# Optimization experiments

Measured on AMD Instinct MI355X. Metric: run time of the kernel, lower is better.

The kernel has to match this reference:

```python
import jax, jax.numpy as jnp
import numpy as np
import math

HEAD_SIZE = 64

def setup_inputs() -> dict:
    key = jax.random.key(0)
    k1, k2, k3 = jax.random.split(key, 3)
    B, nh, T, hs = 2, 16, 2048, HEAD_SIZE
    return {
        "query": jax.random.normal(k1, (B, nh, T, hs), dtype=jnp.float32),
        "key": jax.random.normal(k2, (B, nh, T, hs), dtype=jnp.float32),
        "value": jax.random.normal(k3, (B, nh, T, hs), dtype=jnp.float32),
        "attention_mask": jnp.zeros((B, 1, 1, T), dtype=jnp.float32),
    }

def reference(query, key, value, attention_mask):
    scale = 1.0 / math.sqrt(HEAD_SIZE)
    # [B, nh, T, T] scores
    scores = jnp.einsum("bhqd,bhkd->bhqk", query, key) * scale
    scores = scores + attention_mask
    attn = jax.nn.softmax(scores, axis=-1)
    # [B, nh, T, hs]
    return jnp.einsum("bhqk,bhkd->bhqd", attn, value)
```

## Files before the change

kernel.cpp:

```cpp
#include <hip/hip_runtime.h>
#include <hip/hip_bf16.h>

#define TSEQ 2048
#define DH   64
#define NBH  32
#define KT   32
#define NIT  32

typedef __attribute__((ext_vector_type(8)))  short short8_t;
typedef __attribute__((ext_vector_type(16))) float f32x16;
typedef __attribute__((ext_vector_type(4)))  unsigned short ushort4_t;

#define LOG2E 1.44269504088896340736f
#define MSUB  12.0f

__device__ __forceinline__ unsigned short f2bf(float f) {
    unsigned int u = __float_as_uint(f);
    return (unsigned short)((u + 0x7fffu + ((u >> 16) & 1u)) >> 16);
}

__device__ __forceinline__ unsigned int cvtpk(float lo, float hi) {
    unsigned int r;
    asm("v_cvt_pk_bf16_f32 %0, %1, %2" : "=v"(r) : "v"(lo), "v"(hi));
    return r;
}

__device__ __forceinline__ float exp2r(float x) {
#if __has_builtin(__builtin_amdgcn_exp2f)
    return __builtin_amdgcn_exp2f(x);
#else
    return exp2f(x);
#endif
}

#define GL2L16(g, l) __builtin_amdgcn_global_load_lds( \
    (__attribute__((address_space(1))) void*)(void*)(g), \
    (__attribute__((address_space(3))) void*)(l), 16, 0, 0)

__device__ __forceinline__ unsigned int kswz(unsigned int row, unsigned int cb) {
    return row * 128u + (cb ^ ((row & 7u) << 4));
}
__device__ __forceinline__ unsigned int vswz(unsigned int row, unsigned int cb) {
    return row * 64u + (cb ^ (((row >> 1) & 3u) << 4));
}

__global__ __launch_bounds__(256) void prep_kernel(const float* __restrict__ K,
                                                   unsigned short* __restrict__ Kb,
                                                   const float* __restrict__ V,
                                                   unsigned short* __restrict__ Vt) {
    __shared__ float tile[64][65];
    const int tid = threadIdx.x;
    if (blockIdx.x < 2048) {
        int i = blockIdx.x * 256 + tid;
        const float4* s = reinterpret_cast<const float4*>(K) + (size_t)i * 2;
        float4 a = s[0], b = s[1];
        short8_t o;
        o[0] = (short)f2bf(a.x); o[1] = (short)f2bf(a.y);
        o[2] = (short)f2bf(a.z); o[3] = (short)f2bf(a.w);
        o[4] = (short)f2bf(b.x); o[5] = (short)f2bf(b.y);
        o[6] = (short)f2bf(b.z); o[7] = (short)f2bf(b.w);
        *reinterpret_cast<short8_t*>(Kb + (size_t)i * 8) = o;
        return;
    }
    const int vbid = blockIdx.x - 2048;
    const int bh = vbid >> 5;
    const int t0 = (vbid & 31) * 64;
    const float* src = V + ((size_t)bh * TSEQ + t0) * DH;
#pragma unroll
    for (int it = 0; it < 4; ++it) {
        int idx = tid + it * 256;
        int row = idx >> 4;
        int c   = (idx & 15) * 4;
        float4 v = *reinterpret_cast<const float4*>(src + row * DH + c);
        tile[row][c + 0] = v.x; tile[row][c + 1] = v.y;
        tile[row][c + 2] = v.z; tile[row][c + 3] = v.w;
    }
    __syncthreads();
#pragma unroll
    for (int it = 0; it < 4; ++it) {
        int idx = tid + it * 256;
        int d  = idx >> 4;
        int c  = (idx & 15) * 4;
        ushort4_t o;
        o[0] = f2bf(tile[c + 0][d]); o[1] = f2bf(tile[c + 1][d]);
        o[2] = f2bf(tile[c + 2][d]); o[3] = f2bf(tile[c + 3][d]);
        *reinterpret_cast<ushort4_t*>(Vt + ((size_t)bh * DH + d) * TSEQ + t0 + c) = o;
    }
}

__global__ __launch_bounds__(256, 2) void attn_kernel(const float* __restrict__ Qf,
                                                      const unsigned short* __restrict__ Kb,
                                                      const unsigned short* __restrict__ Vt,
                                                      const float* __restrict__ mask,
                                                      float* __restrict__ out) {
    __shared__ char lds[40960];
    float* smsk = reinterpret_cast<float*>(lds + 32768);

    const int tid  = threadIdx.x;
    const int wave = tid >> 6;
    const int lane = tid & 63;
    const int l31  = lane & 31;
    const int hi   = lane >> 5;
    const int s    = wave >> 1;
    const int qw   = wave & 1;

    const int bid = blockIdx.x;
    const int bh  = (bid & 7) * 4 + (bid >> 7);
    const int qb  = (bid >> 3) & 15;
    const int q0  = qb * 128 + qw * 64;
    const int b   = bh >> 4;

    const char* gKc = reinterpret_cast<const char*>(Kb + (size_t)bh * TSEQ * DH);
    const char* gVc = reinterpret_cast<const char*>(Vt + (size_t)bh * DH * TSEQ);
    const unsigned int kr  = wave * 8 + (lane >> 3);
    const unsigned int kcb = (lane & 7) * 16;
    const unsigned int vd  = wave * 16 + (lane >> 2);
    const unsigned int vcb = (lane & 3) * 16;
    const char* p0 = gKc + (size_t)kr * 128 + (kcb ^ ((kr & 7u) << 4));
    const char* p1 = p0 + (size_t)1024 * 128;
    const char* p2 = gVc + (size_t)vd * 4096 + (vcb ^ (((vd >> 1) & 3u) << 4));
    const char* p3 = p2 + (size_t)1024 * 2;
    const unsigned int lo0 = (wave +  0) * 1024 + lane * 16;
    const unsigned int lo1 = (wave +  4) * 1024 + lane * 16;
    const unsigned int lo2 = (wave +  8) * 1024 + lane * 16;
    const unsigned int lo3 = (wave + 12) * 1024 + lane * 16;

    auto stage = [&](int buf) {
        char* base = lds + buf * 16384;
        GL2L16(p0, base + lo0);
        GL2L16(p1, base + lo1);
        GL2L16(p2, base + lo2);
        GL2L16(p3, base + lo3);
        p0 += KT * 128; p1 += KT * 128; p2 += KT * 2; p3 += KT * 2;
    };

    stage(0);
    stage(1);

    {
        const float4* m4 = reinterpret_cast<const float4*>(mask + (size_t)b * TSEQ);
        float4* s4 = reinterpret_cast<float4*>(smsk);
#pragma unroll
        for (int i = 0; i < 2; ++i) {
            int idx = tid + i * 256;
            float4 v = m4[idx];
            float4 w;
            w.x = v.x * LOG2E - MSUB; w.y = v.y * LOG2E - MSUB;
            w.z = v.z * LOG2E - MSUB; w.w = v.w * LOG2E - MSUB;
            s4[idx] = w;
        }
    }

    const float QS = 0.125f * LOG2E;
    short8_t qfA[4], qfB[4];
#pragma unroll
    for (int qs = 0; qs < 2; ++qs) {
        const float* qrow = Qf + ((size_t)bh * TSEQ + q0 + qs * 32 + l31) * DH;
#pragma unroll
        for (int dc = 0; dc < 4; ++dc) {
            float4 v0 = *reinterpret_cast<const float4*>(qrow + 16 * dc + 8 * hi);
            float4 v1 = *reinterpret_cast<const float4*>(qrow + 16 * dc + 8 * hi + 4);
            union { unsigned int u[4]; short8_t s8; } pk;
            pk.u[0] = cvtpk(v0.x * QS, v0.y * QS);
            pk.u[1] = cvtpk(v0.z * QS, v0.w * QS);
            pk.u[2] = cvtpk(v1.x * QS, v1.y * QS);
            pk.u[3] = cvtpk(v1.z * QS, v1.w * QS);
            if (qs == 0) qfA[dc] = pk.s8; else qfB[dc] = pk.s8;
        }
    }

    f32x16 oA0, oA1, oB0, oB1;
#pragma unroll
    for (int r = 0; r < 16; ++r) { oA0[r] = 0.f; oA1[r] = 0.f; oB0[r] = 0.f; oB1[r] = 0.f; }
    float lA = 0.f, lB = 0.f;

    const char* const cKbase = lds + s * 4096;
    const char* const cVbase = lds + 8192 + s * 4096;
    const int kofs = s * 1024;

    auto do_tile = [&](int cur, int it) {
        const char* cK = cKbase + cur * 16384;
        const char* cV = cVbase + cur * 16384;

        short8_t kf0 = *reinterpret_cast<const short8_t*>(cK + kswz(l31, 16 * hi));
        short8_t kf1 = *reinterpret_cast<const short8_t*>(cK + kswz(l31, 32 + 16 * hi));
        short8_t kf2 = *reinterpret_cast<const short8_t*>(cK + kswz(l31, 64 + 16 * hi));
        short8_t kf3 = *reinterpret_cast<const short8_t*>(cK + kswz(l31, 96 + 16 * hi));

        const float* mb = &smsk[kofs + it * KT + 4 * hi];
        float4 mv0 = *reinterpret_cast<const float4*>(mb);
        float4 mv1 = *reinterpret_cast<const float4*>(mb + 8);
        float4 mv2 = *reinterpret_cast<const float4*>(mb + 16);
        float4 mv3 = *reinterpret_cast<const float4*>(mb + 24);
        f32x16 scA;
        scA[0]  = mv0.x; scA[1]  = mv0.y; scA[2]  = mv0.z; scA[3]  = mv0.w;
        scA[4]  = mv1.x; scA[5]  = mv1.y; scA[6]  = mv1.z; scA[7]  = mv1.w;
        scA[8]  = mv2.x; scA[9]  = mv2.y; scA[10] = mv2.z; scA[11] = mv2.w;
        scA[12] = mv3.x; scA[13] = mv3.y; scA[14] = mv3.z; scA[15] = mv3.w;
        f32x16 scB = scA;

        __builtin_amdgcn_s_setprio(1);
        scA = __builtin_amdgcn_mfma_f32_32x32x16_bf16(kf0, qfA[0], scA, 0, 0, 0);
        scB = __builtin_amdgcn_mfma_f32_32x32x16_bf16(kf0, qfB[0], scB, 0, 0, 0);
        scA = __builtin_amdgcn_mfma_f32_32x32x16_bf16(kf1, qfA[1], scA, 0, 0, 0);
        scB = __builtin_amdgcn_mfma_f32_32x32x16_bf16(kf1, qfB[1], scB, 0, 0, 0);
        scA = __builtin_amdgcn_mfma_f32_32x32x16_bf16(kf2, qfA[2], scA, 0, 0, 0);
        scB = __builtin_amdgcn_mfma_f32_32x32x16_bf16(kf2, qfB[2], scB, 0, 0, 0);
        scA = __builtin_amdgcn_mfma_f32_32x32x16_bf16(kf3, qfA[3], scA, 0, 0, 0);
        scB = __builtin_amdgcn_mfma_f32_32x32x16_bf16(kf3, qfB[3], scB, 0, 0, 0);
        __builtin_amdgcn_s_setprio(0);

        short8_t vf00 = *reinterpret_cast<const short8_t*>(cV + vswz(l31,      16 * hi));
        short8_t vf01 = *reinterpret_cast<const short8_t*>(cV + vswz(32 + l31, 16 * hi));
        short8_t vf10 = *reinterpret_cast<const short8_t*>(cV + vswz(l31,      32 + 16 * hi));
        short8_t vf11 = *reinterpret_cast<const short8_t*>(cV + vswz(32 + l31, 32 + 16 * hi));

#pragma unroll
        for (int c = 0; c < 2; ++c) {
            unsigned int a0, a1, a2, a3, b0, b1, b2, b3;
            {
                float e0 = exp2r(scA[8*c+0]), e1 = exp2r(scA[8*c+1]);
                float e2 = exp2r(scA[8*c+2]), e3 = exp2r(scA[8*c+3]);
                float e4 = exp2r(scA[8*c+4]), e5 = exp2r(scA[8*c+5]);
                float e6 = exp2r(scA[8*c+6]), e7 = exp2r(scA[8*c+7]);
                lA += ((e0+e1)+(e2+e3)) + ((e4+e5)+(e6+e7));
                a0 = cvtpk(e0, e1); a2 = cvtpk(e2, e3);
                a1 = cvtpk(e4, e5); a3 = cvtpk(e6, e7);
            }
            {
                float e0 = exp2r(scB[8*c+0]), e1 = exp2r(scB[8*c+1]);
                float e2 = exp2r(scB[8*c+2]), e3 = exp2r(scB[8*c+3]);
                float e4 = exp2r(scB[8*c+4]), e5 = exp2r(scB[8*c+5]);
                float e6 = exp2r(scB[8*c+6]), e7 = exp2r(scB[8*c+7]);
                lB += ((e0+e1)+(e2+e3)) + ((e4+e5)+(e6+e7));
                b0 = cvtpk(e0, e1); b2 = cvtpk(e2, e3);
                b1 = cvtpk(e4, e5); b3 = cvtpk(e6, e7);
            }
            asm("v_permlane32_swap_b32 %0, %1" : "+v"(a0), "+v"(a1));
            asm("v_permlane32_swap_b32 %0, %1" : "+v"(a2), "+v"(a3));
            asm("v_permlane32_swap_b32 %0, %1" : "+v"(b0), "+v"(b1));
            asm("v_permlane32_swap_b32 %0, %1" : "+v"(b2), "+v"(b3));
            union { unsigned int u[4]; short8_t s8; } pfA, pfB;
            pfA.u[0] = a0; pfA.u[1] = a2; pfA.u[2] = a1; pfA.u[3] = a3;
            pfB.u[0] = b0; pfB.u[1] = b2; pfB.u[2] = b1; pfB.u[3] = b3;
            short8_t vf0 = c ? vf10 : vf00;
            short8_t vf1 = c ? vf11 : vf01;
            __builtin_amdgcn_s_setprio(1);
            oA0 = __builtin_amdgcn_mfma_f32_32x32x16_bf16(vf0, pfA.s8, oA0, 0, 0, 0);
            oB0 = __builtin_amdgcn_mfma_f32_32x32x16_bf16(vf0, pfB.s8, oB0, 0, 0, 0);
            oA1 = __builtin_amdgcn_mfma_f32_32x32x16_bf16(vf1, pfA.s8, oA1, 0, 0, 0);
            oB1 = __builtin_amdgcn_mfma_f32_32x32x16_bf16(vf1, pfB.s8, oB1, 0, 0, 0);
            __builtin_amdgcn_s_setprio(0);
        }
    };

    __syncthreads();

    for (int t = 0; t < NIT - 1; ++t) {
        asm volatile("s_waitcnt vmcnt(4)" ::: "memory");
        __builtin_amdgcn_s_barrier();
        __builtin_amdgcn_sched_barrier(0);
        do_tile(t & 1, t);
        __builtin_amdgcn_sched_barrier(0);
        __builtin_amdgcn_s_barrier();
        __builtin_amdgcn_sched_barrier(0);
        if (t < NIT - 2) stage(t & 1);
    }
    asm volatile("s_waitcnt vmcnt(0)" ::: "memory");
    __builtin_amdgcn_s_barrier();
    __builtin_amdgcn_sched_barrier(0);
    do_tile((NIT - 1) & 1, NIT - 1);

    __syncthreads();

    float lAt = lA + __shfl_xor(lA, 32);
    float lBt = lB + __shfl_xor(lB, 32);
    if (s == 1) {
#pragma unroll
        for (int qs = 0; qs < 2; ++qs) {
            char* wp = lds + qw * 16384 + qs * 8192;
            const f32x16& o0 = qs ? oB0 : oA0;
            const f32x16& o1 = qs ? oB1 : oA1;
#pragma unroll
            for (int i = 0; i < 8; ++i) {
                float4 v;
                if (i < 4) { v.x = o0[4*i]; v.y = o0[4*i+1]; v.z = o0[4*i+2]; v.w = o0[4*i+3]; }
                else       { v.x = o1[4*(i-4)]; v.y = o1[4*(i-4)+1]; v.z = o1[4*(i-4)+2]; v.w = o1[4*(i-4)+3]; }
                *reinterpret_cast<float4*>(wp + lane * 128 + ((i * 16) ^ ((lane & 7u) << 4))) = v;
            }
        }
        if (hi == 0) {
            reinterpret_cast<float*>(lds + 32768 + (qw * 2 + 0) * 128)[l31] = lAt;
            reinterpret_cast<float*>(lds + 32768 + (qw * 2 + 1) * 128)[l31] = lBt;
        }
    }
    __syncthreads();
    if (s == 0) {
#pragma unroll
        for (int qs = 0; qs < 2; ++qs) {
            const char* rp = lds + qw * 16384 + qs * 8192;
            const f32x16& o0 = qs ? oB0 : oA0;
            const f32x16& o1 = qs ? oB1 : oA1;
            float lpart = qs ? lBt : lAt;
            float ltt = lpart + reinterpret_cast<const float*>(lds + 32768 + (qw * 2 + qs) * 128)[l31];
            float inv = 1.0f / ltt;
            float* orow = out + ((size_t)bh * TSEQ + q0 + qs * 32 + l31) * DH;
#pragma unroll
            for (int i = 0; i < 8; ++i) {
                float4 o = *reinterpret_cast<const float4*>(rp + lane * 128 + ((i * 16) ^ ((lane & 7u) << 4)));
                float4 v;
                if (i < 4) {
                    v.x = (o0[4*i]   + o.x) * inv; v.y = (o0[4*i+1] + o.y) * inv;
                    v.z = (o0[4*i+2] + o.z) * inv; v.w = (o0[4*i+3] + o.w) * inv;
                } else {
                    v.x = (o1[4*(i-4)]   + o.x) * inv; v.y = (o1[4*(i-4)+1] + o.y) * inv;
                    v.z = (o1[4*(i-4)+2] + o.z) * inv; v.w = (o1[4*(i-4)+3] + o.w) * inv;
                }
                const int db = i >> 2, rr = i & 3;
                *reinterpret_cast<float4*>(orow + 32 * db + 8 * rr + 4 * hi) = v;
            }
        }
    }
}

extern "C" void kernel_launch(void* const* d_in, const int* in_sizes, int n_in,
                              void* d_out, int out_size, void* d_ws, size_t ws_size,
                              hipStream_t stream) {
    const float* Q    = (const float*)d_in[0];
    const float* K    = (const float*)d_in[1];
    const float* V    = (const float*)d_in[2];
    const float* mask = (const float*)d_in[3];
    float* out = (float*)d_out;

    const size_t N = (size_t)NBH * TSEQ * DH;
    unsigned short* Kb = (unsigned short*)d_ws;
    unsigned short* Vt = Kb + N;

    hipLaunchKernelGGL(prep_kernel, dim3(2048 + 1024), dim3(256), 0, stream, K, Kb, V, Vt);
    hipLaunchKernelGGL(attn_kernel, dim3(16 * NBH), dim3(256), 0, stream,
                       Q, Kb, Vt, mask, out);
}
```

Before: 57.47 us.

## Give each wave private K/V staging buffers and drop per-tile block barriers

Each wave now loads its own K and V tile slices into a private double-buffered LDS region instead of the block cooperatively staging shared buffers. The block-wide s_barrier calls in the main loop are replaced by per-wave vmcnt/lgkmcnt waits, so waves no longer stall on each other every tile. This doubles per-wave global load instructions and raises LDS use from 40KB to 72KB per block, which may limit occupancy to two blocks per CU or fewer.

```diff
diff --git a/kernel.cpp b/kernel.cpp
--- a/kernel.cpp
+++ b/kernel.cpp
@@ -93,8 +93,8 @@
                                                       const unsigned short* __restrict__ Vt,
                                                       const float* __restrict__ mask,
                                                       float* __restrict__ out) {
-    __shared__ char lds[40960];
-    float* smsk = reinterpret_cast<float*>(lds + 32768);
+    __shared__ char lds[73728];
+    float* smsk = reinterpret_cast<float*>(lds + 65536);
 
     const int tid  = threadIdx.x;
     const int wave = tid >> 6;
@@ -112,26 +112,27 @@
 
     const char* gKc = reinterpret_cast<const char*>(Kb + (size_t)bh * TSEQ * DH);
     const char* gVc = reinterpret_cast<const char*>(Vt + (size_t)bh * DH * TSEQ);
-    const unsigned int kr  = wave * 8 + (lane >> 3);
     const unsigned int kcb = (lane & 7) * 16;
-    const unsigned int vd  = wave * 16 + (lane >> 2);
-    const unsigned int vcb = (lane & 3) * 16;
-    const char* p0 = gKc + (size_t)kr * 128 + (kcb ^ ((kr & 7u) << 4));
-    const char* p1 = p0 + (size_t)1024 * 128;
-    const char* p2 = gVc + (size_t)vd * 4096 + (vcb ^ (((vd >> 1) & 3u) << 4));
-    const char* p3 = p2 + (size_t)1024 * 2;
-    const unsigned int lo0 = (wave +  0) * 1024 + lane * 16;
-    const unsigned int lo1 = (wave +  4) * 1024 + lane * 16;
-    const unsigned int lo2 = (wave +  8) * 1024 + lane * 16;
-    const unsigned int lo3 = (wave + 12) * 1024 + lane * 16;
+    const unsigned int vrl = lane >> 2;
+    const char* pK = gKc + (size_t)(s * 1024 + (lane >> 3)) * 128
+                     + (kcb ^ (((lane >> 3) & 7u) << 4));
+    const char* pV = gVc + (size_t)vrl * 4096 + (size_t)(s * 1024) * 2
+                     + (((lane & 3) * 16) ^ (((vrl >> 1) & 3u) << 4));
+    char* const myBase = lds + wave * 16384;
+    char* const dK = myBase + lane * 16;
+    char* const dV = myBase + 4096 + lane * 16;
 
     auto stage = [&](int buf) {
-        char* base = lds + buf * 16384;
-        GL2L16(p0, base + lo0);
-        GL2L16(p1, base + lo1);
-        GL2L16(p2, base + lo2);
-        GL2L16(p3, base + lo3);
-        p0 += KT * 128; p1 += KT * 128; p2 += KT * 2; p3 += KT * 2;
+        const unsigned int bo = buf * 8192;
+        GL2L16(pK + 0,      dK + bo + 0);
+        GL2L16(pK + 1024,   dK + bo + 1024);
+        GL2L16(pK + 2048,   dK + bo + 2048);
+        GL2L16(pK + 3072,   dK + bo + 3072);
+        GL2L16(pV + 0,      dV + bo + 0);
+        GL2L16(pV + 65536,  dV + bo + 1024);
+        GL2L16(pV + 131072, dV + bo + 2048);
+        GL2L16(pV + 196608, dV + bo + 3072);
+        pK += KT * 128; pV += KT * 2;
     };
 
     stage(0);
@@ -174,13 +175,11 @@
     for (int r = 0; r < 16; ++r) { oA0[r] = 0.f; oA1[r] = 0.f; oB0[r] = 0.f; oB1[r] = 0.f; }
     float lA = 0.f, lB = 0.f;
 
-    const char* const cKbase = lds + s * 4096;
-    const char* const cVbase = lds + 8192 + s * 4096;
     const int kofs = s * 1024;
 
-    auto do_tile = [&](int cur, int it) {
-        const char* cK = cKbase + cur * 16384;
-        const char* cV = cVbase + cur * 16384;
+    auto do_tile = [&](const char* bb, int it) {
+        const char* cK = bb;
+        const char* cV = bb + 4096;
 
         short8_t kf0 = *reinterpret_cast<const short8_t*>(cK + kswz(l31, 16 * hi));
         short8_t kf1 = *reinterpret_cast<const short8_t*>(cK + kswz(l31, 32 + 16 * hi));
@@ -256,20 +255,16 @@
 
     __syncthreads();
 
-    for (int t = 0; t < NIT - 1; ++t) {
-        asm volatile("s_waitcnt vmcnt(4)" ::: "memory");
-        __builtin_amdgcn_s_barrier();
+    for (int t = 0; t < NIT; ++t) {
+        if (t < NIT - 1) { asm volatile("s_waitcnt vmcnt(8)" ::: "memory"); }
+        else             { asm volatile("s_waitcnt vmcnt(0)" ::: "memory"); }
         __builtin_amdgcn_sched_barrier(0);
-        do_tile(t & 1, t);
+        do_tile(myBase + (t & 1) * 8192, t);
         __builtin_amdgcn_sched_barrier(0);
-        __builtin_amdgcn_s_barrier();
+        asm volatile("s_waitcnt lgkmcnt(0)" ::: "memory");
         __builtin_amdgcn_sched_barrier(0);
         if (t < NIT - 2) stage(t & 1);
     }
-    asm volatile("s_waitcnt vmcnt(0)" ::: "memory");
-    __builtin_amdgcn_s_barrier();
-    __builtin_amdgcn_sched_barrier(0);
-    do_tile((NIT - 1) & 1, NIT - 1);
 
     __syncthreads();
 
@@ -290,8 +285,8 @@
             }
         }
         if (hi == 0) {
-            reinterpret_cast<float*>(lds + 32768 + (qw * 2 + 0) * 128)[l31] = lAt;
-            reinterpret_cast<float*>(lds + 32768 + (qw * 2 + 1) * 128)[l31] = lBt;
+            reinterpret_cast<float*>(lds + 65536 + (qw * 2 + 0) * 128)[l31] = lAt;
+            reinterpret_cast<float*>(lds + 65536 + (qw * 2 + 1) * 128)[l31] = lBt;
         }
     }
     __syncthreads();
@@ -302,7 +297,7 @@
             const f32x16& o0 = qs ? oB0 : oA0;
             const f32x16& o1 = qs ? oB1 : oA1;
             float lpart = qs ? lBt : lAt;
-            float ltt = lpart + reinterpret_cast<const float*>(lds + 32768 + (qw * 2 + qs) * 128)[l31];
+            float ltt = lpart + reinterpret_cast<const float*>(lds + 65536 + (qw * 2 + qs) * 128)[l31];
             float inv = 1.0f / ltt;
             float* orow = out + ((size_t)bh * TSEQ + q0 + qs * 32 + l31) * DH;
 #pragma unroll
```

After: 61.10 us. 1.06x slower.
